# Optimization experiments

Hardware: AMD Instinct MI355X
Metric: run time of the kernel (lower is better)

The kernel has to match this reference:

```python
import jax, jax.numpy as jnp
import numpy as np

N, E = 50000, 640000
DIN, DH, DOUT = 128, 256, 128


def _glorot(k, i, o):
    return jax.random.normal(k, (i, o), jnp.float32) / np.sqrt(i)


def setup_inputs() -> dict:
    key = jax.random.key(0)
    ks = jax.random.split(key, 12)
    return {
        "x": jax.random.normal(ks[0], (N, DIN), jnp.float32),
        "edge_index": jax.random.randint(ks[1], (2, E), 0, N, dtype=jnp.int32),
        # SAGEConv 1: in -> hidden (lin_l on aggregated w/ bias, lin_r on root)
        "W1l": _glorot(ks[2], DIN, DH), "b1l": jnp.zeros((DH,), jnp.float32), "W1r": _glorot(ks[3], DIN, DH),
        "g1": jnp.ones((DH,), jnp.float32), "be1": jnp.zeros((DH,), jnp.float32),
        # skip projection (in != hidden)
        "Wsk": _glorot(ks[4], DIN, DH), "bsk": jnp.zeros((DH,), jnp.float32),
        # SAGEConv 2: hidden -> hidden
        "W2l": _glorot(ks[5], DH, DH), "b2l": jnp.zeros((DH,), jnp.float32), "W2r": _glorot(ks[6], DH, DH),
        "g2": jnp.ones((DH,), jnp.float32), "be2": jnp.zeros((DH,), jnp.float32),
        # SAGEConv 3: hidden -> out
        "W3l": _glorot(ks[7], DH, DOUT), "b3l": jnp.zeros((DOUT,), jnp.float32), "W3r": _glorot(ks[8], DH, DOUT),
    }


def _sage_conv(x, src, dst, Wl, bl, Wr, n):
    # mean aggregation of source features into destination nodes
    msg = x[src]                                                 # [E, d]
    agg = jax.ops.segment_sum(msg, dst, num_segments=n)          # [N, d]
    cnt = jax.ops.segment_sum(jnp.ones((src.shape[0],), x.dtype), dst, num_segments=n)
    agg = agg / jnp.maximum(cnt, 1.0)[:, None]
    return agg @ Wl + bl + x @ Wr


def _layernorm(x, g, b):
    mu = jnp.mean(x, axis=-1, keepdims=True)
    var = jnp.mean((x - mu) ** 2, axis=-1, keepdims=True)
    return (x - mu) * jax.lax.rsqrt(var + 1e-5) * g + b


def reference(x, edge_index, W1l, b1l, W1r, g1, be1, Wsk, bsk,
              W2l, b2l, W2r, g2, be2, W3l, b3l, W3r):
    src, dst = edge_index[0], edge_index[1]
    n = x.shape[0]
    # layer 0: conv -> LN -> relu -> (dropout p=0, eval) -> skip via projection
    h = _sage_conv(x, src, dst, W1l, b1l, W1r, n)
    h = jax.nn.relu(_layernorm(h, g1, be1))
    h = h + (x @ Wsk + bsk)
    # layer 1: conv -> LN -> relu -> residual add (shapes match)
    h2 = _sage_conv(h, src, dst, W2l, b2l, W2r, n)
    h2 = jax.nn.relu(_layernorm(h2, g2, be2)) + h
    # final conv (no norm/act)
    return _sage_conv(h2, src, dst, W3l, b3l, W3r, n)
```

## Files before the change

kernel.cpp:

```cpp
#include <hip/hip_runtime.h>


typedef float floatx4 __attribute__((ext_vector_type(4)));
typedef float floatx2 __attribute__((ext_vector_type(2)));
typedef short bf16x8 __attribute__((ext_vector_type(8)));

__device__ inline unsigned short f2bf(float f) {
    unsigned u = __float_as_uint(f);
    unsigned r = (u + 0x7fffu + ((u >> 16) & 1u)) >> 16;
    return (unsigned short)r;
}
__device__ inline float bf2f_lo(unsigned v) { return __uint_as_float(v << 16); }
__device__ inline float bf2f_hi(unsigned v) { return __uint_as_float(v & 0xffff0000u); }

__device__ inline void gl_lds16(const void* g, void* l) {
    __builtin_amdgcn_global_load_lds((const __attribute__((address_space(1))) unsigned int*)g,
                                     (__attribute__((address_space(3))) unsigned int*)l,
                                     16, 0, 0);
}

__global__ void hist_kernel(const int* __restrict__ dst, int* __restrict__ cnt, int E) {
    int i = blockIdx.x * blockDim.x + threadIdx.x;
    if (i < E) atomicAdd(&cnt[dst[i]], 1);
}

#define SCAN_CHUNK 2048

__global__ __launch_bounds__(256) void scan_blocksums(const int* __restrict__ cnt,
                                                      int* __restrict__ bsum, int N) {
    __shared__ int sh[256];
    int t = threadIdx.x;
    int base = blockIdx.x * SCAN_CHUNK + t * 8;
    int s = 0;
#pragma unroll
    for (int i = 0; i < 8; i++) {
        int idx = base + i;
        if (idx < N) s += cnt[idx];
    }
    sh[t] = s;
    __syncthreads();
    for (int off = 1; off < 256; off <<= 1) {
        int v = (t >= off) ? sh[t - off] : 0;
        __syncthreads();
        sh[t] += v;
        __syncthreads();
    }
    if (t == 255) bsum[blockIdx.x] = sh[255];
}

__global__ __launch_bounds__(256) void scan_bsums(const int* __restrict__ bsum,
                                                  int* __restrict__ boff, int NB,
                                                  int* __restrict__ rowptr, int N, int E) {
    __shared__ int sh[256];
    int t = threadIdx.x;
    int v = (t < NB) ? bsum[t] : 0;
    sh[t] = v;
    __syncthreads();
    for (int off = 1; off < 256; off <<= 1) {
        int u = (t >= off) ? sh[t - off] : 0;
        __syncthreads();
        sh[t] += u;
        __syncthreads();
    }
    if (t < NB) boff[t] = sh[t] - v;
    if (t == 0) rowptr[N] = E;
}

__global__ __launch_bounds__(256) void scan_final(const int* __restrict__ cnt,
                                                  const int* __restrict__ boff,
                                                  int* __restrict__ rowptr,
                                                  int* __restrict__ cursor,
                                                  float* __restrict__ invdeg, int N) {
    __shared__ int sh[256];
    int t = threadIdx.x;
    int base = blockIdx.x * SCAN_CHUNK + t * 8;
    int c[8];
    int s = 0;
#pragma unroll
    for (int i = 0; i < 8; i++) {
        int idx = base + i;
        c[i] = (idx < N) ? cnt[idx] : 0;
        s += c[i];
    }
    sh[t] = s;
    __syncthreads();
    for (int off = 1; off < 256; off <<= 1) {
        int v = (t >= off) ? sh[t - off] : 0;
        __syncthreads();
        sh[t] += v;
        __syncthreads();
    }
    int run = boff[blockIdx.x] + sh[t] - s;
#pragma unroll
    for (int i = 0; i < 8; i++) {
        int idx = base + i;
        if (idx < N) {
            rowptr[idx] = run;
            cursor[idx] = run;
            invdeg[idx] = 1.0f / (float)(c[i] > 1 ? c[i] : 1);
            run += c[i];
        }
    }
}

__global__ void scatter_kernel(const int* __restrict__ src, const int* __restrict__ dst,
                               int* __restrict__ cursor, int* __restrict__ col, int E) {
    int i = blockIdx.x * blockDim.x + threadIdx.x;
    if (i < E) {
        int p = atomicAdd(&cursor[dst[i]], 1);
        col[p] = src[i];
    }
}

__global__ void prep_weights(const float* __restrict__ W1l, const float* __restrict__ W1r,
                             const float* __restrict__ Wsk, const float* __restrict__ W2l,
                             const float* __restrict__ W2r, const float* __restrict__ W3l,
                             const float* __restrict__ W3r, const float* __restrict__ b1l,
                             const float* __restrict__ bsk,
                             unsigned short* __restrict__ WtC, unsigned short* __restrict__ Wt2,
                             unsigned short* __restrict__ Wt3, float* __restrict__ biasC) {
    int i = blockIdx.x * blockDim.x + threadIdx.x;
    if (i < 32768) {
        int k = i >> 8, n = i & 255;
        WtC[n * 256 + k] = f2bf(W1l[i]);
    } else if (i < 65536) {
        int j = i - 32768, k = j >> 8, n = j & 255;
        WtC[n * 256 + 128 + k] = f2bf(W1r[j]);
    } else if (i < 98304) {
        int j = i - 65536, k = j >> 8, n = j & 255;
        WtC[(256 + n) * 256 + 128 + k] = f2bf(Wsk[j]);
    } else if (i < 131072) {
        int j = i - 98304, k = j >> 8, n = j & 255;
        WtC[(256 + n) * 256 + k] = 0;
    } else if (i < 196608) {
        int j = i - 131072, k = j >> 8, n = j & 255;
        Wt2[n * 512 + k] = f2bf(W2l[j]);
    } else if (i < 262144) {
        int j = i - 196608, k = j >> 8, n = j & 255;
        Wt2[n * 512 + 256 + k] = f2bf(W2r[j]);
    } else if (i < 294912) {
        int j = i - 262144, k = j >> 7, n = j & 127;
        Wt3[n * 256 + k] = f2bf(W3l[j]);
    } else if (i < 327680) {
        int j = i - 294912, k = j >> 7, n = j & 127;
        Wt3[(128 + n) * 256 + k] = f2bf(W3r[j]);
    } else if (i < 328192) {
        int j = i - 327680;
        biasC[j] = (j < 256) ? b1l[j] : bsk[j - 256];
    }
}

__global__ void cvt_x2(const float* __restrict__ x, unsigned short* __restrict__ A1cat,
                       unsigned char* __restrict__ X8, int total32) {
    int i = blockIdx.x * blockDim.x + threadIdx.x;
    if (i >= total32) return;
    int r = i >> 5, c4 = (i & 31) * 4;
    float4 v = *(const float4*)(x + (size_t)r * 128 + c4);
    ushort4 o;
    o.x = f2bf(v.x); o.y = f2bf(v.y); o.z = f2bf(v.z); o.w = f2bf(v.w);
    *(ushort4*)(A1cat + (size_t)r * 256 + 128 + c4) = o;
    unsigned wpk = 0;
    wpk = __builtin_amdgcn_cvt_pk_fp8_f32(v.x, v.y, wpk, false);
    wpk = __builtin_amdgcn_cvt_pk_fp8_f32(v.z, v.w, wpk, true);
    *(unsigned*)(X8 + (size_t)r * 128 + c4) = wpk;
}

__device__ inline void accum_fp8(uint2 v, float m, float* a) {
    floatx2 p;
    p = __builtin_amdgcn_cvt_pk_f32_fp8(v.x, false); a[0] = fmaf(m, p.x, a[0]); a[1] = fmaf(m, p.y, a[1]);
    p = __builtin_amdgcn_cvt_pk_f32_fp8(v.x, true);  a[2] = fmaf(m, p.x, a[2]); a[3] = fmaf(m, p.y, a[3]);
    p = __builtin_amdgcn_cvt_pk_f32_fp8(v.y, false); a[4] = fmaf(m, p.x, a[4]); a[5] = fmaf(m, p.y, a[5]);
    p = __builtin_amdgcn_cvt_pk_f32_fp8(v.y, true);  a[6] = fmaf(m, p.x, a[6]); a[7] = fmaf(m, p.y, a[7]);
}

__global__ __launch_bounds__(256) void agg_fp8_128(const int* __restrict__ rowptr,
                                                   const int* __restrict__ col,
                                                   const float* __restrict__ invdeg,
                                                   const unsigned char* __restrict__ X8,
                                                   unsigned short* __restrict__ out, int ostride, int N) {
    int wid = (blockIdx.x * blockDim.x + threadIdx.x) >> 6;
    int lane = threadIdx.x & 63;
    if (wid >= N) return;
    int q = lane >> 4;
    int sub = lane & 15;
    const unsigned char* Xo = X8 + sub * 8;
    int s = rowptr[wid], e = rowptr[wid + 1];
    float a[8] = {0.f, 0.f, 0.f, 0.f, 0.f, 0.f, 0.f, 0.f};
    for (int j = s + q; j < e; j += 16) {
        int j1 = (j + 4 < e) ? j + 4 : j;
        int j2 = (j + 8 < e) ? j + 8 : j;
        int j3 = (j + 12 < e) ? j + 12 : j;
        float m1 = (j + 4 < e) ? 1.f : 0.f;
        float m2 = (j + 8 < e) ? 1.f : 0.f;
        float m3 = (j + 12 < e) ? 1.f : 0.f;
        int c0 = col[j], c1 = col[j1], c2 = col[j2], c3 = col[j3];
        uint2 v0 = *(const uint2*)(Xo + (size_t)c0 * 128);
        uint2 v1 = *(const uint2*)(Xo + (size_t)c1 * 128);
        uint2 v2 = *(const uint2*)(Xo + (size_t)c2 * 128);
        uint2 v3 = *(const uint2*)(Xo + (size_t)c3 * 128);
        accum_fp8(v0, 1.f, a);
        accum_fp8(v1, m1, a);
        accum_fp8(v2, m2, a);
        accum_fp8(v3, m3, a);
    }
#pragma unroll
    for (int i = 0; i < 8; i++) {
        a[i] += __shfl_xor(a[i], 16, 64);
        a[i] += __shfl_xor(a[i], 32, 64);
    }
    if (q == 0) {
        float inv = invdeg[wid];
        uint4 o;
        o.x = (unsigned)f2bf(a[0] * inv) | ((unsigned)f2bf(a[1] * inv) << 16);
        o.y = (unsigned)f2bf(a[2] * inv) | ((unsigned)f2bf(a[3] * inv) << 16);
        o.z = (unsigned)f2bf(a[4] * inv) | ((unsigned)f2bf(a[5] * inv) << 16);
        o.w = (unsigned)f2bf(a[6] * inv) | ((unsigned)f2bf(a[7] * inv) << 16);
        *(uint4*)(out + (size_t)wid * ostride + sub * 8) = o;
    }
}

__global__ __launch_bounds__(256) void agg_fp8_256(const int* __restrict__ rowptr,
                                                   const int* __restrict__ col,
                                                   const float* __restrict__ invdeg,
                                                   const unsigned char* __restrict__ H8,
                                                   unsigned short* __restrict__ out, int ostride, int N) {
    int wid = (blockIdx.x * blockDim.x + threadIdx.x) >> 6;
    int lane = threadIdx.x & 63;
    if (wid >= N) return;
    int half = lane >> 5;
    int sub = lane & 31;
    const unsigned char* Ho = H8 + sub * 8;
    int s = rowptr[wid], e = rowptr[wid + 1];
    float a[8] = {0.f, 0.f, 0.f, 0.f, 0.f, 0.f, 0.f, 0.f};
    for (int j = s + half; j < e; j += 8) {
        int j1 = (j + 2 < e) ? j + 2 : j;
        int j2 = (j + 4 < e) ? j + 4 : j;
        int j3 = (j + 6 < e) ? j + 6 : j;
        float m1 = (j + 2 < e) ? 1.f : 0.f;
        float m2 = (j + 4 < e) ? 1.f : 0.f;
        float m3 = (j + 6 < e) ? 1.f : 0.f;
        int c0 = col[j], c1 = col[j1], c2 = col[j2], c3 = col[j3];
        uint2 v0 = *(const uint2*)(Ho + (size_t)c0 * 256);
        uint2 v1 = *(const uint2*)(Ho + (size_t)c1 * 256);
        uint2 v2 = *(const uint2*)(Ho + (size_t)c2 * 256);
        uint2 v3 = *(const uint2*)(Ho + (size_t)c3 * 256);
        accum_fp8(v0, 1.f, a);
        accum_fp8(v1, m1, a);
        accum_fp8(v2, m2, a);
        accum_fp8(v3, m3, a);
    }
#pragma unroll
    for (int i = 0; i < 8; i++) a[i] += __shfl_xor(a[i], 32, 64);
    if (half == 0) {
        float inv = invdeg[wid];
        uint4 o;
        o.x = (unsigned)f2bf(a[0] * inv) | ((unsigned)f2bf(a[1] * inv) << 16);
        o.y = (unsigned)f2bf(a[2] * inv) | ((unsigned)f2bf(a[3] * inv) << 16);
        o.z = (unsigned)f2bf(a[4] * inv) | ((unsigned)f2bf(a[5] * inv) << 16);
        o.w = (unsigned)f2bf(a[6] * inv) | ((unsigned)f2bf(a[7] * inv) << 16);
        *(uint4*)(out + (size_t)wid * ostride + sub * 8) = o;
    }
}

__global__ __launch_bounds__(256) void agg_final_v3(const int* __restrict__ rowptr,
                                                    const int* __restrict__ col,
                                                    const float* __restrict__ invdeg,
                                                    const unsigned short* __restrict__ T,
                                                    const float* __restrict__ R,
                                                    float* __restrict__ out, int N) {
    int wid = (blockIdx.x * blockDim.x + threadIdx.x) >> 6;
    int lane = threadIdx.x & 63;
    if (wid >= N) return;
    int half = lane >> 5;
    int sub = lane & 31;
    const unsigned short* To = T + sub * 4;
    int s = rowptr[wid], e = rowptr[wid + 1];
    float a0 = 0.f, a1 = 0.f, a2 = 0.f, a3 = 0.f;
    for (int j = s + half; j < e; j += 8) {
        int j1 = (j + 2 < e) ? j + 2 : j;
        int j2 = (j + 4 < e) ? j + 4 : j;
        int j3 = (j + 6 < e) ? j + 6 : j;
        float m1 = (j + 2 < e) ? 1.f : 0.f;
        float m2 = (j + 4 < e) ? 1.f : 0.f;
        float m3 = (j + 6 < e) ? 1.f : 0.f;
        int c0 = col[j], c1 = col[j1], c2 = col[j2], c3 = col[j3];
        uint2 v0 = *(const uint2*)(To + (size_t)c0 * 128);
        uint2 v1 = *(const uint2*)(To + (size_t)c1 * 128);
        uint2 v2 = *(const uint2*)(To + (size_t)c2 * 128);
        uint2 v3 = *(const uint2*)(To + (size_t)c3 * 128);
        a0 += bf2f_lo(v0.x); a1 += bf2f_hi(v0.x); a2 += bf2f_lo(v0.y); a3 += bf2f_hi(v0.y);
        a0 = fmaf(m1, bf2f_lo(v1.x), a0); a1 = fmaf(m1, bf2f_hi(v1.x), a1);
        a2 = fmaf(m1, bf2f_lo(v1.y), a2); a3 = fmaf(m1, bf2f_hi(v1.y), a3);
        a0 = fmaf(m2, bf2f_lo(v2.x), a0); a1 = fmaf(m2, bf2f_hi(v2.x), a1);
        a2 = fmaf(m2, bf2f_lo(v2.y), a2); a3 = fmaf(m2, bf2f_hi(v2.y), a3);
        a0 = fmaf(m3, bf2f_lo(v3.x), a0); a1 = fmaf(m3, bf2f_hi(v3.x), a1);
        a2 = fmaf(m3, bf2f_lo(v3.y), a2); a3 = fmaf(m3, bf2f_hi(v3.y), a3);
    }
    a0 += __shfl_xor(a0, 32, 64);
    a1 += __shfl_xor(a1, 32, 64);
    a2 += __shfl_xor(a2, 32, 64);
    a3 += __shfl_xor(a3, 32, 64);
    if (half == 0) {
        float inv = invdeg[wid];
        float4 r = *(const float4*)(R + (size_t)wid * 128 + sub * 4);
        float4 o;
        o.x = a0 * inv + r.x;
        o.y = a1 * inv + r.y;
        o.z = a2 * inv + r.z;
        o.w = a3 * inv + r.w;
        *(float4*)(out + (size_t)wid * 128 + sub * 4) = o;
    }
}

template <int KIT, int NPAN, int MODE>
__global__ __launch_bounds__(512) void gemm_fused(
    const unsigned short* __restrict__ A, int lda,
    const unsigned short* __restrict__ B, int ldb,
    const float* __restrict__ bias,
    const float* __restrict__ gamma, const float* __restrict__ beta,
    const unsigned short* __restrict__ resid,
    unsigned short* __restrict__ outb,
    unsigned char* __restrict__ h8,
    float* __restrict__ outf, int M) {
    constexpr int COLS = NPAN * 256;
    constexpr int LNW = COLS + 8;
    constexpr int STAGE_E = 128 * 64;
    constexpr int STAGE_F = 2 * STAGE_E / 2;
    constexpr int SMEM_F = (STAGE_F > 32 * LNW) ? STAGE_F : 32 * LNW;
    __shared__ __align__(16) float smemf[SMEM_F];
    unsigned short* sbase = (unsigned short*)smemf;

    int t = threadIdx.x;
    int lane = t & 63, w = t >> 6;
    int bm = blockIdx.x * 128;
    int wm = (w & 1) * 64, wn = (w >> 1) * 64;
    int m16 = lane & 15, kq = lane >> 4;

    floatx4 acc[NPAN][4][4];
#pragma unroll
    for (int p = 0; p < NPAN; p++)
#pragma unroll
        for (int i = 0; i < 4; i++)
#pragma unroll
            for (int j = 0; j < 4; j++) acc[p][i][j] = (floatx4){0.f, 0.f, 0.f, 0.f};

    const int s_row0 = t >> 3;
    const int s_j = t & 7;

    auto stage = [&](int kt, int bsel) {
        unsigned short* s = sbase + bsel * STAGE_E;
        int k0 = kt * 64;
#pragma unroll
        for (int i = 0; i < 2; i++) {
            int row = s_row0 + i * 64;
            int kc = s_j ^ (row & 7);
            int rowA = bm + row;
            if (rowA > M - 1) rowA = M - 1;
            gl_lds16(A + (size_t)rowA * lda + k0 + kc * 8, (void*)&s[(size_t)(i * 512 + t) * 8]);
        }
    };

    stage(0, 0);
    __syncthreads();
    for (int kt = 0; kt < KIT; kt++) {
        if (kt + 1 < KIT) stage(kt + 1, (kt & 1) ^ 1);
        const unsigned short* sA = sbase + (kt & 1) * STAGE_E;
#pragma unroll
        for (int ks = 0; ks < 2; ks++) {
            int kcl = (ks << 2) | kq;
            bf16x8 af[4];
#pragma unroll
            for (int mi = 0; mi < 4; mi++)
                af[mi] = *(const bf16x8*)&sA[(wm + mi * 16 + m16) * 64 + (kcl ^ (m16 & 7)) * 8];
#pragma unroll
            for (int p = 0; p < NPAN; p++) {
                if (MODE == 0 && p == 1 && kt * 64 < 128) continue;
                const unsigned short* Bp = B + (size_t)(wn + p * 256) * ldb + kt * 64;
                bf16x8 bf[4];
#pragma unroll
                for (int ni = 0; ni < 4; ni++)
                    bf[ni] = *(const bf16x8*)&Bp[(size_t)(ni * 16 + m16) * ldb + kcl * 8];
#pragma unroll
                for (int mi = 0; mi < 4; mi++)
#pragma unroll
                    for (int ni = 0; ni < 4; ni++)
                        acc[p][mi][ni] =
                            __builtin_amdgcn_mfma_f32_16x16x32_bf16(af[mi], bf[ni], acc[p][mi][ni], 0, 0, 0);
            }
        }
        __syncthreads();
    }

    float* lnb = smemf;
    int c4 = lane * 4;
    float4 bu = {0.f, 0.f, 0.f, 0.f}, bs = {0.f, 0.f, 0.f, 0.f};
    float4 gv = {0.f, 0.f, 0.f, 0.f}, bv = {0.f, 0.f, 0.f, 0.f};
    float4 b3 = {0.f, 0.f, 0.f, 0.f};
    if (MODE == 0) {
        bu = *(const float4*)&bias[c4];
        bs = *(const float4*)&bias[256 + c4];
        gv = *(const float4*)&gamma[c4];
        bv = *(const float4*)&beta[c4];
    } else if (MODE == 1) {
        bu = *(const float4*)&bias[c4];
        gv = *(const float4*)&gamma[c4];
        bv = *(const float4*)&beta[c4];
    } else {
        if (lane >= 32) b3 = *(const float4*)&bias[c4 - 128];
    }

#pragma unroll
    for (int g4 = 0; g4 < 4; g4++) {
        if (wm == (g4 >> 1) * 64) {
            int mi0 = (g4 & 1) * 2;
#pragma unroll
            for (int p = 0; p < NPAN; p++)
#pragma unroll
                for (int mm = 0; mm < 2; mm++)
#pragma unroll
                    for (int ni = 0; ni < 4; ni++)
#pragma unroll
                        for (int r = 0; r < 4; r++)
                            lnb[(mm * 16 + kq * 4 + r) * LNW + wn + p * 256 + ni * 16 + m16] =
                                acc[p][mi0 + mm][ni][r];
        }
        __syncthreads();
#pragma unroll
        for (int rr = 0; rr < 4; rr++) {
            int lrow = w * 4 + rr;
            int grow = bm + g4 * 32 + lrow;
            bool valid = grow < M;
            float4 u = *(const float4*)&lnb[lrow * LNW + c4];
            if (MODE <= 1) {
                u.x += bu.x; u.y += bu.y; u.z += bu.z; u.w += bu.w;
                float s1 = (u.x + u.y) + (u.z + u.w);
                float s2 = (u.x * u.x + u.y * u.y) + (u.z * u.z + u.w * u.w);
#pragma unroll
                for (int off = 1; off < 64; off <<= 1) {
                    s1 += __shfl_xor(s1, off, 64);
                    s2 += __shfl_xor(s2, off, 64);
                }
                float mu = s1 * (1.f / 256.f);
                float var = s2 * (1.f / 256.f) - mu * mu;
                float rs = rsqrtf(var + 1e-5f);
                float a0, a1, a2, a3;
                if (MODE == 0) {
                    float4 sv = *(const float4*)&lnb[lrow * LNW + 256 + c4];
                    a0 = sv.x + bs.x; a1 = sv.y + bs.y; a2 = sv.z + bs.z; a3 = sv.w + bs.w;
                } else {
                    int gr = valid ? grow : M - 1;
                    uint2 hv = *(const uint2*)(resid + (size_t)gr * 512 + c4);
                    a0 = bf2f_lo(hv.x); a1 = bf2f_hi(hv.x); a2 = bf2f_lo(hv.y); a3 = bf2f_hi(hv.y);
                }
                float o0 = fmaxf((u.x - mu) * rs * gv.x + bv.x, 0.f) + a0;
                float o1 = fmaxf((u.y - mu) * rs * gv.y + bv.y, 0.f) + a1;
                float o2 = fmaxf((u.z - mu) * rs * gv.z + bv.z, 0.f) + a2;
                float o3 = fmaxf((u.w - mu) * rs * gv.w + bv.w, 0.f) + a3;
                if (valid) {
                    ushort4 o;
                    o.x = f2bf(o0); o.y = f2bf(o1); o.z = f2bf(o2); o.w = f2bf(o3);
                    *(ushort4*)(outb + (size_t)grow * 512 + c4) = o;
                    if (MODE == 0) {
                        unsigned wpk = 0;
                        wpk = __builtin_amdgcn_cvt_pk_fp8_f32(o0, o1, wpk, false);
                        wpk = __builtin_amdgcn_cvt_pk_fp8_f32(o2, o3, wpk, true);
                        *(unsigned*)(h8 + (size_t)grow * 256 + c4) = wpk;
                    }
                }
            } else {
                if (valid) {
                    if (lane < 32) {
                        ushort4 o;
                        o.x = f2bf(u.x); o.y = f2bf(u.y); o.z = f2bf(u.z); o.w = f2bf(u.w);
                        *(ushort4*)(outb + (size_t)grow * 128 + c4) = o;
                    } else {
                        float4 o;
                        o.x = u.x + b3.x; o.y = u.y + b3.y; o.z = u.z + b3.z; o.w = u.w + b3.w;
                        *(float4*)(outf + (size_t)grow * 128 + (c4 - 128)) = o;
                    }
                }
            }
        }
        __syncthreads();
    }
}

extern "C" void kernel_launch(void* const* d_in, const int* in_sizes, int n_in,
                              void* d_out, int out_size, void* d_ws, size_t ws_size,
                              hipStream_t stream) {
    const float* x   = (const float*)d_in[0];
    const int*   ei  = (const int*)d_in[1];
    const float* W1l = (const float*)d_in[2];
    const float* b1l = (const float*)d_in[3];
    const float* W1r = (const float*)d_in[4];
    const float* g1  = (const float*)d_in[5];
    const float* be1 = (const float*)d_in[6];
    const float* Wsk = (const float*)d_in[7];
    const float* bsk = (const float*)d_in[8];
    const float* W2l = (const float*)d_in[9];
    const float* b2l = (const float*)d_in[10];
    const float* W2r = (const float*)d_in[11];
    const float* g2  = (const float*)d_in[12];
    const float* be2 = (const float*)d_in[13];
    const float* W3l = (const float*)d_in[14];
    const float* b3l = (const float*)d_in[15];
    const float* W3r = (const float*)d_in[16];

    const int N = in_sizes[0] / 128;
    const int E = in_sizes[1] / 2;
    const int* src = ei;
    const int* dst = ei + E;

    char* p = (char*)d_ws;
    auto alloc = [&](size_t bytes) {
        void* r = (void*)p;
        p += (bytes + 255) & ~(size_t)255;
        return r;
    };
    int*   cnt    = (int*)alloc(sizeof(int) * N);
    int*   rowptr = (int*)alloc(sizeof(int) * (N + 1));
    int*   cursor = (int*)alloc(sizeof(int) * N);
    float* invdeg = (float*)alloc(sizeof(float) * N);
    int*   col    = (int*)alloc(sizeof(int) * E);
    int*   bsum   = (int*)alloc(sizeof(int) * 256);
    int*   boff   = (int*)alloc(sizeof(int) * 256);
    unsigned short* A1cat = (unsigned short*)alloc(sizeof(short) * (size_t)N * 256);
    unsigned short* A2cat = (unsigned short*)alloc(sizeof(short) * (size_t)N * 512);
    float* r3 = (float*)alloc(sizeof(float) * (size_t)N * 128);
    unsigned char* H8 = (unsigned char*)alloc((size_t)N * 256);
    unsigned char* X8 = (unsigned char*)alloc((size_t)N * 128);
    unsigned short* WtC = (unsigned short*)alloc(sizeof(short) * 512 * 256);
    unsigned short* Wt2 = (unsigned short*)alloc(sizeof(short) * 256 * 512);
    unsigned short* Wt3 = (unsigned short*)alloc(sizeof(short) * 256 * 256);
    float* biasC = (float*)alloc(sizeof(float) * 512);
    unsigned short* t3 = A1cat;

    hipMemsetAsync(cnt, 0, sizeof(int) * N, stream);
    hist_kernel<<<(E + 255) / 256, 256, 0, stream>>>(dst, cnt, E);
    int NB = (N + SCAN_CHUNK - 1) / SCAN_CHUNK;
    scan_blocksums<<<NB, 256, 0, stream>>>(cnt, bsum, N);
    scan_bsums<<<1, 256, 0, stream>>>(bsum, boff, NB, rowptr, N, E);
    scan_final<<<NB, 256, 0, stream>>>(cnt, boff, rowptr, cursor, invdeg, N);
    scatter_kernel<<<(E + 255) / 256, 256, 0, stream>>>(src, dst, cursor, col, E);

    prep_weights<<<(328192 + 255) / 256, 256, 0, stream>>>(W1l, W1r, Wsk, W2l, W2r, W3l, W3r,
                                                           b1l, bsk, WtC, Wt2, Wt3, biasC);
    cvt_x2<<<((N * 32) + 255) / 256, 256, 0, stream>>>(x, A1cat, X8, N * 32);

    int aggBlocks = (N + 3) / 4;
    int mBlocks = (N + 127) / 128;

    agg_fp8_128<<<aggBlocks, 256, 0, stream>>>(rowptr, col, invdeg, X8, A1cat, 256, N);
    gemm_fused<4, 2, 0><<<mBlocks, 512, 0, stream>>>(A1cat, 256, WtC, 256, biasC, g1, be1,
                                                     nullptr, A2cat + 256, H8, nullptr, N);

    agg_fp8_256<<<aggBlocks, 256, 0, stream>>>(rowptr, col, invdeg, H8, A2cat, 512, N);
    gemm_fused<8, 1, 1><<<mBlocks, 512, 0, stream>>>(A2cat, 512, Wt2, 512, b2l, g2, be2,
                                                     A2cat + 256, A2cat, nullptr, nullptr, N);

    gemm_fused<4, 1, 2><<<mBlocks, 512, 0, stream>>>(A2cat, 512, Wt3, 256, b3l, nullptr, nullptr,
                                                     nullptr, t3, nullptr, r3, N);
    agg_final_v3<<<aggBlocks, 256, 0, stream>>>(rowptr, col, invdeg, t3, r3, (float*)d_out, N);
}
```

Measured before the change: 388.3 us.

## Retile fused GEMMs to 64-row blocks with one 64-column strip per wave

Replaces the 128-row block tile (2x4 wave grid, two column panels per wave) with 64-row tiles where each wave owns a 64-column strip across all rows. Block size now depends on output width: 512 threads for the 512-wide first layer, 256 for the others. This halves the accumulators per wave and doubles the grid, aiming for better occupancy and load balance across CUs. The cost is less reuse of each A tile and B fragment per block, and more global B reads overall.

Result: slower. 400.2 us (+3.1%).

```diff
diff --git a/kernel.cpp b/kernel.cpp
--- a/kernel.cpp
+++ b/kernel.cpp
@@ -312,8 +312,8 @@
     }
 }
 
-template <int KIT, int NPAN, int MODE>
-__global__ __launch_bounds__(512) void gemm_fused(
+template <int KIT, int NW, int MODE>
+__global__ __launch_bounds__(NW * 64) void gemm_v6(
     const unsigned short* __restrict__ A, int lda,
     const unsigned short* __restrict__ B, int ldb,
     const float* __restrict__ bias,
@@ -322,41 +322,36 @@
     unsigned short* __restrict__ outb,
     unsigned char* __restrict__ h8,
     float* __restrict__ outf, int M) {
-    constexpr int COLS = NPAN * 256;
+    constexpr int COLS = NW * 64;
     constexpr int LNW = COLS + 8;
-    constexpr int STAGE_E = 128 * 64;
-    constexpr int STAGE_F = 2 * STAGE_E / 2;
-    constexpr int SMEM_F = (STAGE_F > 32 * LNW) ? STAGE_F : 32 * LNW;
+    constexpr int STAGE_E = 64 * 64;
+    constexpr int SMEM_F = (STAGE_E > 16 * LNW) ? STAGE_E : 16 * LNW;
     __shared__ __align__(16) float smemf[SMEM_F];
     unsigned short* sbase = (unsigned short*)smemf;
 
     int t = threadIdx.x;
     int lane = t & 63, w = t >> 6;
-    int bm = blockIdx.x * 128;
-    int wm = (w & 1) * 64, wn = (w >> 1) * 64;
+    int bm = blockIdx.x * 64;
+    int wn = w * 64;
     int m16 = lane & 15, kq = lane >> 4;
 
-    floatx4 acc[NPAN][4][4];
-#pragma unroll
-    for (int p = 0; p < NPAN; p++)
-#pragma unroll
-        for (int i = 0; i < 4; i++)
-#pragma unroll
-            for (int j = 0; j < 4; j++) acc[p][i][j] = (floatx4){0.f, 0.f, 0.f, 0.f};
-
-    const int s_row0 = t >> 3;
-    const int s_j = t & 7;
+    floatx4 acc[4][4];
+#pragma unroll
+    for (int i = 0; i < 4; i++)
+#pragma unroll
+        for (int j = 0; j < 4; j++) acc[i][j] = (floatx4){0.f, 0.f, 0.f, 0.f};
 
     auto stage = [&](int kt, int bsel) {
         unsigned short* s = sbase + bsel * STAGE_E;
         int k0 = kt * 64;
 #pragma unroll
-        for (int i = 0; i < 2; i++) {
-            int row = s_row0 + i * 64;
-            int kc = s_j ^ (row & 7);
+        for (int i = 0; i < 512 / (NW * 64); i++) {
+            int idx = i * (NW * 64) + t;
+            int row = idx >> 3, j = idx & 7;
+            int kc = j ^ (row & 7);
             int rowA = bm + row;
             if (rowA > M - 1) rowA = M - 1;
-            gl_lds16(A + (size_t)rowA * lda + k0 + kc * 8, (void*)&s[(size_t)(i * 512 + t) * 8]);
+            gl_lds16(A + (size_t)rowA * lda + k0 + kc * 8, (void*)&s[(size_t)idx * 8]);
         }
     };
 
@@ -365,17 +360,16 @@
     for (int kt = 0; kt < KIT; kt++) {
         if (kt + 1 < KIT) stage(kt + 1, (kt & 1) ^ 1);
         const unsigned short* sA = sbase + (kt & 1) * STAGE_E;
-#pragma unroll
-        for (int ks = 0; ks < 2; ks++) {
-            int kcl = (ks << 2) | kq;
-            bf16x8 af[4];
-#pragma unroll
-            for (int mi = 0; mi < 4; mi++)
-                af[mi] = *(const bf16x8*)&sA[(wm + mi * 16 + m16) * 64 + (kcl ^ (m16 & 7)) * 8];
-#pragma unroll
-            for (int p = 0; p < NPAN; p++) {
-                if (MODE == 0 && p == 1 && kt * 64 < 128) continue;
-                const unsigned short* Bp = B + (size_t)(wn + p * 256) * ldb + kt * 64;
+        bool active = !(MODE == 0 && wn >= 256 && kt < 2);
+        if (active) {
+#pragma unroll
+            for (int ks = 0; ks < 2; ks++) {
+                int kcl = (ks << 2) | kq;
+                bf16x8 af[4];
+#pragma unroll
+                for (int mi = 0; mi < 4; mi++)
+                    af[mi] = *(const bf16x8*)&sA[(mi * 16 + m16) * 64 + (kcl ^ (m16 & 7)) * 8];
+                const unsigned short* Bp = B + (size_t)wn * ldb + kt * 64;
                 bf16x8 bf[4];
 #pragma unroll
                 for (int ni = 0; ni < 4; ni++)
@@ -384,8 +378,8 @@
                 for (int mi = 0; mi < 4; mi++)
 #pragma unroll
                     for (int ni = 0; ni < 4; ni++)
-                        acc[p][mi][ni] =
-                            __builtin_amdgcn_mfma_f32_16x16x32_bf16(af[mi], bf[ni], acc[p][mi][ni], 0, 0, 0);
+                        acc[mi][ni] =
+                            __builtin_amdgcn_mfma_f32_16x16x32_bf16(af[mi], bf[ni], acc[mi][ni], 0, 0, 0);
             }
         }
         __syncthreads();
@@ -409,26 +403,19 @@
         if (lane >= 32) b3 = *(const float4*)&bias[c4 - 128];
     }
 
-#pragma unroll
-    for (int g4 = 0; g4 < 4; g4++) {
-        if (wm == (g4 >> 1) * 64) {
-            int mi0 = (g4 & 1) * 2;
-#pragma unroll
-            for (int p = 0; p < NPAN; p++)
-#pragma unroll
-                for (int mm = 0; mm < 2; mm++)
-#pragma unroll
-                    for (int ni = 0; ni < 4; ni++)
-#pragma unroll
-                        for (int r = 0; r < 4; r++)
-                            lnb[(mm * 16 + kq * 4 + r) * LNW + wn + p * 256 + ni * 16 + m16] =
-                                acc[p][mi0 + mm][ni][r];
-        }
-        __syncthreads();
-#pragma unroll
-        for (int rr = 0; rr < 4; rr++) {
-            int lrow = w * 4 + rr;
-            int grow = bm + g4 * 32 + lrow;
+    constexpr int RPW = 16 / NW;
+#pragma unroll
+    for (int g = 0; g < 4; g++) {
+#pragma unroll
+        for (int ni = 0; ni < 4; ni++)
+#pragma unroll
+            for (int r = 0; r < 4; r++)
+                lnb[(kq * 4 + r) * LNW + wn + ni * 16 + m16] = acc[g][ni][r];
+        __syncthreads();
+#pragma unroll
+        for (int rr = 0; rr < RPW; rr++) {
+            int lrow = w * RPW + rr;
+            int grow = bm + g * 16 + lrow;
             bool valid = grow < M;
             float4 u = *(const float4*)&lnb[lrow * LNW + c4];
             if (MODE <= 1) {
@@ -548,17 +535,17 @@
     cvt_x2<<<((N * 32) + 255) / 256, 256, 0, stream>>>(x, A1cat, X8, N * 32);
 
     int aggBlocks = (N + 3) / 4;
-    int mBlocks = (N + 127) / 128;
+    int m64 = (N + 63) / 64;
 
     agg_fp8_128<<<aggBlocks, 256, 0, stream>>>(rowptr, col, invdeg, X8, A1cat, 256, N);
-    gemm_fused<4, 2, 0><<<mBlocks, 512, 0, stream>>>(A1cat, 256, WtC, 256, biasC, g1, be1,
-                                                     nullptr, A2cat + 256, H8, nullptr, N);
+    gemm_v6<4, 8, 0><<<m64, 512, 0, stream>>>(A1cat, 256, WtC, 256, biasC, g1, be1,
+                                              nullptr, A2cat + 256, H8, nullptr, N);
 
     agg_fp8_256<<<aggBlocks, 256, 0, stream>>>(rowptr, col, invdeg, H8, A2cat, 512, N);
-    gemm_fused<8, 1, 1><<<mBlocks, 512, 0, stream>>>(A2cat, 512, Wt2, 512, b2l, g2, be2,
-                                                     A2cat + 256, A2cat, nullptr, nullptr, N);
-
-    gemm_fused<4, 1, 2><<<mBlocks, 512, 0, stream>>>(A2cat, 512, Wt3, 256, b3l, nullptr, nullptr,
-                                                     nullptr, t3, nullptr, r3, N);
+    gemm_v6<8, 4, 1><<<m64, 256, 0, stream>>>(A2cat, 512, Wt2, 512, b2l, g2, be2,
+                                              A2cat + 256, A2cat, nullptr, nullptr, N);
+
+    gemm_v6<4, 4, 2><<<m64, 256, 0, stream>>>(A2cat, 512, Wt3, 256, b3l, nullptr, nullptr,
+                                              nullptr, t3, nullptr, r3, N);
     agg_final_v3<<<aggBlocks, 256, 0, stream>>>(rowptr, col, invdeg, t3, r3, (float*)d_out, N);
 }
```

## Split aggregation kernels across feature-column chunks with more edge-parallel lanes

Applied to the files above, without the earlier changes.

The three gather/mean aggregation kernels now split the feature dimension into 64-byte column chunks via a second grid dimension. Each wave handles one node's chunk with 8 lanes per row and 8 edge groups, so more edges are in flight per wave. The aim is more memory-level parallelism and fewer idle lanes on low-degree nodes. In exchange, the col indices are re-read once per chunk, rows are fetched in smaller pieces, and an extra shuffle reduction step is added.

Measured after the change: 469.9 us. +21.0%, slower.

```diff
diff --git a/kernel.cpp b/kernel.cpp
--- a/kernel.cpp
+++ b/kernel.cpp
@@ -173,31 +173,33 @@
     p = __builtin_amdgcn_cvt_pk_f32_fp8(v.y, true);  a[6] = fmaf(m, p.x, a[6]); a[7] = fmaf(m, p.y, a[7]);
 }
 
-__global__ __launch_bounds__(256) void agg_fp8_128(const int* __restrict__ rowptr,
-                                                   const int* __restrict__ col,
-                                                   const float* __restrict__ invdeg,
-                                                   const unsigned char* __restrict__ X8,
-                                                   unsigned short* __restrict__ out, int ostride, int N) {
+template <int RSB>
+__global__ __launch_bounds__(256) void agg_fp8_c(const int* __restrict__ rowptr,
+                                                 const int* __restrict__ col,
+                                                 const float* __restrict__ invdeg,
+                                                 const unsigned char* __restrict__ T8,
+                                                 unsigned short* __restrict__ out, int ostride, int N) {
     int wid = (blockIdx.x * blockDim.x + threadIdx.x) >> 6;
     int lane = threadIdx.x & 63;
     if (wid >= N) return;
-    int q = lane >> 4;
-    int sub = lane & 15;
-    const unsigned char* Xo = X8 + sub * 8;
+    int co = blockIdx.y * 64;
+    int sub = lane & 7;
+    int g = lane >> 3;
+    const unsigned char* To = T8 + co + sub * 8;
     int s = rowptr[wid], e = rowptr[wid + 1];
     float a[8] = {0.f, 0.f, 0.f, 0.f, 0.f, 0.f, 0.f, 0.f};
-    for (int j = s + q; j < e; j += 16) {
-        int j1 = (j + 4 < e) ? j + 4 : j;
-        int j2 = (j + 8 < e) ? j + 8 : j;
-        int j3 = (j + 12 < e) ? j + 12 : j;
-        float m1 = (j + 4 < e) ? 1.f : 0.f;
-        float m2 = (j + 8 < e) ? 1.f : 0.f;
-        float m3 = (j + 12 < e) ? 1.f : 0.f;
+    for (int j = s + g; j < e; j += 32) {
+        int j1 = (j + 8 < e) ? j + 8 : j;
+        int j2 = (j + 16 < e) ? j + 16 : j;
+        int j3 = (j + 24 < e) ? j + 24 : j;
+        float m1 = (j + 8 < e) ? 1.f : 0.f;
+        float m2 = (j + 16 < e) ? 1.f : 0.f;
+        float m3 = (j + 24 < e) ? 1.f : 0.f;
         int c0 = col[j], c1 = col[j1], c2 = col[j2], c3 = col[j3];
-        uint2 v0 = *(const uint2*)(Xo + (size_t)c0 * 128);
-        uint2 v1 = *(const uint2*)(Xo + (size_t)c1 * 128);
-        uint2 v2 = *(const uint2*)(Xo + (size_t)c2 * 128);
-        uint2 v3 = *(const uint2*)(Xo + (size_t)c3 * 128);
+        uint2 v0 = *(const uint2*)(To + (size_t)c0 * RSB);
+        uint2 v1 = *(const uint2*)(To + (size_t)c1 * RSB);
+        uint2 v2 = *(const uint2*)(To + (size_t)c2 * RSB);
+        uint2 v3 = *(const uint2*)(To + (size_t)c3 * RSB);
         accum_fp8(v0, 1.f, a);
         accum_fp8(v1, m1, a);
         accum_fp8(v2, m2, a);
@@ -205,84 +207,43 @@
     }
 #pragma unroll
     for (int i = 0; i < 8; i++) {
+        a[i] += __shfl_xor(a[i], 8, 64);
         a[i] += __shfl_xor(a[i], 16, 64);
         a[i] += __shfl_xor(a[i], 32, 64);
     }
-    if (q == 0) {
+    if (g == 0) {
         float inv = invdeg[wid];
         uint4 o;
         o.x = (unsigned)f2bf(a[0] * inv) | ((unsigned)f2bf(a[1] * inv) << 16);
         o.y = (unsigned)f2bf(a[2] * inv) | ((unsigned)f2bf(a[3] * inv) << 16);
         o.z = (unsigned)f2bf(a[4] * inv) | ((unsigned)f2bf(a[5] * inv) << 16);
         o.w = (unsigned)f2bf(a[6] * inv) | ((unsigned)f2bf(a[7] * inv) << 16);
-        *(uint4*)(out + (size_t)wid * ostride + sub * 8) = o;
-    }
-}
-
-__global__ __launch_bounds__(256) void agg_fp8_256(const int* __restrict__ rowptr,
-                                                   const int* __restrict__ col,
-                                                   const float* __restrict__ invdeg,
-                                                   const unsigned char* __restrict__ H8,
-                                                   unsigned short* __restrict__ out, int ostride, int N) {
+        *(uint4*)(out + (size_t)wid * ostride + co + sub * 8) = o;
+    }
+}
+
+__global__ __launch_bounds__(256) void agg_fin_c(const int* __restrict__ rowptr,
+                                                 const int* __restrict__ col,
+                                                 const float* __restrict__ invdeg,
+                                                 const unsigned short* __restrict__ T,
+                                                 const float* __restrict__ R,
+                                                 float* __restrict__ out, int N) {
     int wid = (blockIdx.x * blockDim.x + threadIdx.x) >> 6;
     int lane = threadIdx.x & 63;
     if (wid >= N) return;
-    int half = lane >> 5;
-    int sub = lane & 31;
-    const unsigned char* Ho = H8 + sub * 8;
-    int s = rowptr[wid], e = rowptr[wid + 1];
-    float a[8] = {0.f, 0.f, 0.f, 0.f, 0.f, 0.f, 0.f, 0.f};
-    for (int j = s + half; j < e; j += 8) {
-        int j1 = (j + 2 < e) ? j + 2 : j;
-        int j2 = (j + 4 < e) ? j + 4 : j;
-        int j3 = (j + 6 < e) ? j + 6 : j;
-        float m1 = (j + 2 < e) ? 1.f : 0.f;
-        float m2 = (j + 4 < e) ? 1.f : 0.f;
-        float m3 = (j + 6 < e) ? 1.f : 0.f;
-        int c0 = col[j], c1 = col[j1], c2 = col[j2], c3 = col[j3];
-        uint2 v0 = *(const uint2*)(Ho + (size_t)c0 * 256);
-        uint2 v1 = *(const uint2*)(Ho + (size_t)c1 * 256);
-        uint2 v2 = *(const uint2*)(Ho + (size_t)c2 * 256);
-        uint2 v3 = *(const uint2*)(Ho + (size_t)c3 * 256);
-        accum_fp8(v0, 1.f, a);
-        accum_fp8(v1, m1, a);
-        accum_fp8(v2, m2, a);
-        accum_fp8(v3, m3, a);
-    }
-#pragma unroll
-    for (int i = 0; i < 8; i++) a[i] += __shfl_xor(a[i], 32, 64);
-    if (half == 0) {
-        float inv = invdeg[wid];
-        uint4 o;
-        o.x = (unsigned)f2bf(a[0] * inv) | ((unsigned)f2bf(a[1] * inv) << 16);
-        o.y = (unsigned)f2bf(a[2] * inv) | ((unsigned)f2bf(a[3] * inv) << 16);
-        o.z = (unsigned)f2bf(a[4] * inv) | ((unsigned)f2bf(a[5] * inv) << 16);
-        o.w = (unsigned)f2bf(a[6] * inv) | ((unsigned)f2bf(a[7] * inv) << 16);
-        *(uint4*)(out + (size_t)wid * ostride + sub * 8) = o;
-    }
-}
-
-__global__ __launch_bounds__(256) void agg_final_v3(const int* __restrict__ rowptr,
-                                                    const int* __restrict__ col,
-                                                    const float* __restrict__ invdeg,
-                                                    const unsigned short* __restrict__ T,
-                                                    const float* __restrict__ R,
-                                                    float* __restrict__ out, int N) {
-    int wid = (blockIdx.x * blockDim.x + threadIdx.x) >> 6;
-    int lane = threadIdx.x & 63;
-    if (wid >= N) return;
-    int half = lane >> 5;
-    int sub = lane & 31;
-    const unsigned short* To = T + sub * 4;
+    int co2 = blockIdx.y * 32;
+    int sub = lane & 7;
+    int g = lane >> 3;
+    const unsigned short* To = T + co2 + sub * 4;
     int s = rowptr[wid], e = rowptr[wid + 1];
     float a0 = 0.f, a1 = 0.f, a2 = 0.f, a3 = 0.f;
-    for (int j = s + half; j < e; j += 8) {
-        int j1 = (j + 2 < e) ? j + 2 : j;
-        int j2 = (j + 4 < e) ? j + 4 : j;
-        int j3 = (j + 6 < e) ? j + 6 : j;
-        float m1 = (j + 2 < e) ? 1.f : 0.f;
-        float m2 = (j + 4 < e) ? 1.f : 0.f;
-        float m3 = (j + 6 < e) ? 1.f : 0.f;
+    for (int j = s + g; j < e; j += 32) {
+        int j1 = (j + 8 < e) ? j + 8 : j;
+        int j2 = (j + 16 < e) ? j + 16 : j;
+        int j3 = (j + 24 < e) ? j + 24 : j;
+        float m1 = (j + 8 < e) ? 1.f : 0.f;
+        float m2 = (j + 16 < e) ? 1.f : 0.f;
+        float m3 = (j + 24 < e) ? 1.f : 0.f;
         int c0 = col[j], c1 = col[j1], c2 = col[j2], c3 = col[j3];
         uint2 v0 = *(const uint2*)(To + (size_t)c0 * 128);
         uint2 v1 = *(const uint2*)(To + (size_t)c1 * 128);
@@ -296,19 +257,22 @@
         a0 = fmaf(m3, bf2f_lo(v3.x), a0); a1 = fmaf(m3, bf2f_hi(v3.x), a1);
         a2 = fmaf(m3, bf2f_lo(v3.y), a2); a3 = fmaf(m3, bf2f_hi(v3.y), a3);
     }
-    a0 += __shfl_xor(a0, 32, 64);
-    a1 += __shfl_xor(a1, 32, 64);
-    a2 += __shfl_xor(a2, 32, 64);
-    a3 += __shfl_xor(a3, 32, 64);
-    if (half == 0) {
+#pragma unroll
+    for (int off = 8; off < 64; off <<= 1) {
+        a0 += __shfl_xor(a0, off, 64);
+        a1 += __shfl_xor(a1, off, 64);
+        a2 += __shfl_xor(a2, off, 64);
+        a3 += __shfl_xor(a3, off, 64);
+    }
+    if (g == 0) {
         float inv = invdeg[wid];
-        float4 r = *(const float4*)(R + (size_t)wid * 128 + sub * 4);
+        float4 r = *(const float4*)(R + (size_t)wid * 128 + co2 + sub * 4);
         float4 o;
         o.x = a0 * inv + r.x;
         o.y = a1 * inv + r.y;
         o.z = a2 * inv + r.z;
         o.w = a3 * inv + r.w;
-        *(float4*)(out + (size_t)wid * 128 + sub * 4) = o;
+        *(float4*)(out + (size_t)wid * 128 + co2 + sub * 4) = o;
     }
 }
 
@@ -550,15 +514,15 @@
     int aggBlocks = (N + 3) / 4;
     int mBlocks = (N + 127) / 128;
 
-    agg_fp8_128<<<aggBlocks, 256, 0, stream>>>(rowptr, col, invdeg, X8, A1cat, 256, N);
+    agg_fp8_c<128><<<dim3(aggBlocks, 2), 256, 0, stream>>>(rowptr, col, invdeg, X8, A1cat, 256, N);
     gemm_fused<4, 2, 0><<<mBlocks, 512, 0, stream>>>(A1cat, 256, WtC, 256, biasC, g1, be1,
                                                      nullptr, A2cat + 256, H8, nullptr, N);
 
-    agg_fp8_256<<<aggBlocks, 256, 0, stream>>>(rowptr, col, invdeg, H8, A2cat, 512, N);
+    agg_fp8_c<256><<<dim3(aggBlocks, 4), 256, 0, stream>>>(rowptr, col, invdeg, H8, A2cat, 512, N);
     gemm_fused<8, 1, 1><<<mBlocks, 512, 0, stream>>>(A2cat, 512, Wt2, 512, b2l, g2, be2,
                                                      A2cat + 256, A2cat, nullptr, nullptr, N);
 
     gemm_fused<4, 1, 2><<<mBlocks, 512, 0, stream>>>(A2cat, 512, Wt3, 256, b3l, nullptr, nullptr,
                                                      nullptr, t3, nullptr, r3, N);
-    agg_final_v3<<<aggBlocks, 256, 0, stream>>>(rowptr, col, invdeg, t3, r3, (float*)d_out, N);
-}
+    agg_fin_c<<<dim3(aggBlocks, 4), 256, 0, stream>>>(rowptr, col, invdeg, t3, r3, (float*)d_out, N);
+}
```
